# Performance work log

Measured on AMD Instinct MI355X. Metric: run time of the kernel, lower is better.

Reference implementation:

```python
import jax, jax.numpy as jnp
import numpy as np

QMAX = 127.0  # int8 symmetric range


def _quantize(t):
    # per-tensor symmetric int8 quantization
    scale = jnp.maximum(jnp.max(jnp.abs(t)) / QMAX, 1e-8)
    q = jnp.clip(jnp.round(t / scale), -QMAX, QMAX)
    return q, scale


def setup_inputs() -> dict:
    key = jax.random.key(0)
    kx, kw, kb = jax.random.split(key, 3)
    x = jax.random.normal(kx, (32, 128, 56, 56), dtype=jnp.float32)
    weight = jax.random.normal(kw, (256, 128, 3, 3), dtype=jnp.float32) * 0.05
    bias = jax.random.normal(kb, (256,), dtype=jnp.float32) * 0.05
    return {"x": x, "weight": weight, "bias": bias}


def reference(x, weight, bias):
    # Quantize activations and weights to int8 grid (values held in fp32;
    # products are exact small integers, matching int32 GEMM accumulation).
    qx, sx = _quantize(x)
    qw, sw = _quantize(weight)
    # im2col GEMM conv == standard conv on quantized values, int accumulate.
    acc = jax.lax.conv_general_dilated(
        qx, qw,
        window_strides=(1, 1),
        padding=((1, 1), (1, 1)),
        rhs_dilation=(1, 1),
        dimension_numbers=("NCHW", "OIHW", "NCHW"),
    )
    # Dequantize and add bias.
    out = acc * (sx * sw) + bias[None, :, None, None]
    return out
```

## Files before the change

### kernel.cpp

```cpp
#include <hip/hip_runtime.h>
#include <hip/hip_bf16.h>


typedef int v4i __attribute__((ext_vector_type(4)));

#define NBATCH 32
#define CIN    128
#define HW     56
#define PIX    (HW*HW)
#define COUT   256
#define XTOT   (NBATCH*CIN*PIX)
#define WTOT   (COUT*CIN*9)

template <int ITERS>
__global__ __launch_bounds__(256) void absmax_part_kernel(
    const float* __restrict__ in, float* __restrict__ partial)
{
    const float4* in4 = (const float4*)in;
    const int t      = blockIdx.x * 256 + threadIdx.x;
    const int stride = gridDim.x * 256;
    float m = 0.f;
#pragma unroll
    for (int k = 0; k < ITERS; ++k) {
        float4 v = in4[t + k * stride];
        m = fmaxf(m, fmaxf(fmaxf(fabsf(v.x), fabsf(v.y)),
                           fmaxf(fabsf(v.z), fabsf(v.w))));
    }
#pragma unroll
    for (int off = 32; off >= 1; off >>= 1)
        m = fmaxf(m, __shfl_xor(m, off, 64));
    __shared__ float wmax[4];
    const int lane = threadIdx.x & 63, wid = threadIdx.x >> 6;
    if (lane == 0) wmax[wid] = m;
    __syncthreads();
    if (threadIdx.x == 0)
        partial[blockIdx.x] =
            fmaxf(fmaxf(wmax[0], wmax[1]), fmaxf(wmax[2], wmax[3]));
}

__global__ __launch_bounds__(256) void finalize_kernel(
    const float* __restrict__ px, const float* __restrict__ pw,
    float* __restrict__ scales)
{
    const int tid = threadIdx.x;
    float mxv = 0.f, mwv = 0.f;
#pragma unroll
    for (int k = 0; k < 4; ++k) {
        int i = k * 256 + tid;
        if (i < 896) mxv = fmaxf(mxv, px[i]);
    }
    if (tid < 72) mwv = pw[tid];
#pragma unroll
    for (int off = 32; off >= 1; off >>= 1) {
        mxv = fmaxf(mxv, __shfl_xor(mxv, off, 64));
        mwv = fmaxf(mwv, __shfl_xor(mwv, off, 64));
    }
    __shared__ float sx[4], sw[4];
    const int lane = tid & 63, wid = tid >> 6;
    if (lane == 0) { sx[wid] = mxv; sw[wid] = mwv; }
    __syncthreads();
    if (tid == 0) {
        float fx = fmaxf(fmaxf(sx[0], sx[1]), fmaxf(sx[2], sx[3]));
        float fw = fmaxf(fmaxf(sw[0], sw[1]), fmaxf(sw[2], sw[3]));
        scales[0] = fmaxf(fx / 127.0f, 1e-8f);
        scales[1] = fmaxf(fw / 127.0f, 1e-8f);
    }
}

__global__ void quant_w_kernel(const float* __restrict__ w,
                               const float* __restrict__ scales,
                               signed char* __restrict__ qw) {
    float s = scales[1];
    int idx = blockIdx.x * blockDim.x + threadIdx.x;
    if (idx >= WTOT) return;
    int o   = idx / (CIN * 9);
    int rem = idx % (CIN * 9);
    int c   = rem / 9;
    int khw = rem % 9;
    float q = rintf(w[idx] / s);
    q = fminf(127.0f, fmaxf(-127.0f, q));
    qw[khw * (COUT * CIN) + o * CIN + c] = (signed char)(int)q;
}

__global__ __launch_bounds__(256) void quant_x_kernel(const float* __restrict__ x,
                                                      const float* __restrict__ scales,
                                                      signed char* __restrict__ qx) {
    __shared__ signed char lds[32 * 132];
    float s = scales[0];
    const int n   = blockIdx.y;
    const int p0  = blockIdx.x * 32;
    const int tid = threadIdx.x;
#pragma unroll
    for (int i = 0; i < 4; ++i) {
        int idx = i * 256 + tid;
        int c   = idx >> 3;
        int pq  = idx & 7;
        float4 v = *(const float4*)&x[((size_t)(n * CIN + c)) * PIX + p0 + pq * 4];
        float qv[4] = {v.x, v.y, v.z, v.w};
#pragma unroll
        for (int j = 0; j < 4; ++j) {
            float q = rintf(qv[j] / s);
            q = fminf(127.0f, fmaxf(-127.0f, q));
            lds[(pq * 4 + j) * 132 + c] = (signed char)(int)q;
        }
    }
    __syncthreads();
#pragma unroll
    for (int i = 0; i < 4; ++i) {
        int idx = i * 256 + tid;
        int pp  = idx >> 5;
        int cw  = (idx & 31) * 4;
        *(int*)&qx[((size_t)(n * PIX + p0 + pp)) * CIN + cw] =
            *(const int*)&lds[pp * 132 + cw];
    }
}

__global__ __launch_bounds__(256) void conv_kernel(
    const signed char* __restrict__ qx,
    const signed char* __restrict__ qw,
    const float* __restrict__ bias,
    const float* __restrict__ scales,
    float* __restrict__ out)
{
    __shared__ signed char lds[192 * 128];
    const int tid  = threadIdx.x;
    const int lane = tid & 63;
    const int wid  = tid >> 6;
    const int prow = lane & 15;
    const int klo  = lane >> 4;

    const int m0 = blockIdx.x * 64;
    const int n  = m0 / PIX;
    const int p0 = m0 % PIX;

    const size_t xbase = (size_t)n * PIX * CIN;
#pragma unroll
    for (int it = 0; it < 6; ++it) {
        int chunk = it * 256 + tid;
        int r  = chunk >> 3;
        int cb = (chunk & 7) * 16;
        int p  = p0 - 57 + r;
        p = min(max(p, 0), PIX - 1);
        v4i v = *(const v4i*)(qx + xbase + (size_t)p * CIN + (cb ^ ((r & 7) << 4)));
        *(v4i*)&lds[r * 128 + cb] = v;
    }
    __syncthreads();

    v4i acc[4][4] = {};
    const v4i vzero = {0, 0, 0, 0};

    int hh[4], ww[4], rbase[4];
#pragma unroll
    for (int s = 0; s < 4; ++s) {
        int i = s * 16 + prow;
        int p = p0 + i;
        hh[s] = p / HW;
        ww[s] = p % HW;
        rbase[s] = i + 57;
    }

#pragma unroll
    for (int dh = -1; dh <= 1; ++dh) {
#pragma unroll
        for (int dw = -1; dw <= 1; ++dw) {
            const int khw = (dh + 1) * 3 + (dw + 1);
            const signed char* bsrc = qw + (size_t)khw * (COUT * CIN);
#pragma unroll
            for (int kc = 0; kc < 2; ++kc) {
                const int col = kc * 64 + klo * 16;
                v4i b[4];
#pragma unroll
                for (int t = 0; t < 4; ++t) {
                    int ch = wid * 64 + t * 16 + prow;
                    b[t] = *(const v4i*)(bsrc + (size_t)ch * CIN + col);
                }
                v4i a[4];
#pragma unroll
                for (int s = 0; s < 4; ++s) {
                    bool valid = ((unsigned)(hh[s] + dh) < (unsigned)HW) &&
                                 ((unsigned)(ww[s] + dw) < (unsigned)HW);
                    int r = rbase[s] + dh * HW + dw;
                    v4i av = *(const v4i*)&lds[r * 128 + (col ^ ((r & 7) << 4))];
                    a[s] = valid ? av : vzero;
                }
#pragma unroll
                for (int s = 0; s < 4; ++s)
#pragma unroll
                    for (int t = 0; t < 4; ++t)
                        acc[s][t] = __builtin_amdgcn_mfma_i32_16x16x64_i8(
                            a[s], b[t], acc[s][t], 0, 0, 0);
            }
        }
    }

    const float comb = scales[0] * scales[1];
    const size_t obase = (size_t)n * COUT * PIX;
#pragma unroll
    for (int t = 0; t < 4; ++t) {
        int ch = wid * 64 + t * 16 + prow;
        float bs = bias[ch];
#pragma unroll
        for (int s = 0; s < 4; ++s) {
            int p = p0 + s * 16 + klo * 4;
            float4 v;
            v.x = (float)acc[s][t].x * comb + bs;
            v.y = (float)acc[s][t].y * comb + bs;
            v.z = (float)acc[s][t].z * comb + bs;
            v.w = (float)acc[s][t].w * comb + bs;
            *(float4*)&out[obase + (size_t)ch * PIX + p] = v;
        }
    }
}

extern "C" void kernel_launch(void* const* d_in, const int* in_sizes, int n_in,
                              void* d_out, int out_size, void* d_ws, size_t ws_size,
                              hipStream_t stream) {
    const float* x    = (const float*)d_in[0];
    const float* w    = (const float*)d_in[1];
    const float* bias = (const float*)d_in[2];
    float* out = (float*)d_out;

    float*       scales = (float*)d_ws;
    float*       px     = (float*)((char*)d_ws + 1024);
    float*       pw     = (float*)((char*)d_ws + 4608);
    signed char* qx     = (signed char*)d_ws + 8192;
    signed char* qw     = qx + (size_t)XTOT;

    absmax_part_kernel<14><<<896, 256, 0, stream>>>(x, px);
    absmax_part_kernel<4><<<72, 256, 0, stream>>>(w, pw);
    finalize_kernel<<<1, 256, 0, stream>>>(px, pw, scales);
    quant_w_kernel<<<WTOT / 256, 256, 0, stream>>>(w, scales, qw);
    quant_x_kernel<<<dim3(98, 32), 256, 0, stream>>>(x, scales, qx);
    conv_kernel<<<1568, 256, 0, stream>>>(qx, qw, bias, scales, out);
}
```

Before: 226.3 us.

## Split conv output channels across blocks with padded LDS halo and prefetched weights

The conv kernel now splits the 256 output channels into two halves per block, doubling the grid and halving each wave's accumulator count. Occupancy is raised via launch bounds. The input tile is staged in LDS as a zero-padded 58-wide halo, which removes the per-tap boundary checks. Weight fragments are software-prefetched one step ahead. The x absmax reduction also runs on twice as many blocks with fewer iterations each. The trade is that each input tile is loaded twice, once per channel half, and LDS per block grows.

```diff
diff --git a/kernel.cpp b/kernel.cpp
--- a/kernel.cpp
+++ b/kernel.cpp
@@ -45,10 +45,8 @@
     const int tid = threadIdx.x;
     float mxv = 0.f, mwv = 0.f;
 #pragma unroll
-    for (int k = 0; k < 4; ++k) {
-        int i = k * 256 + tid;
-        if (i < 896) mxv = fmaxf(mxv, px[i]);
-    }
+    for (int k = 0; k < 7; ++k)
+        mxv = fmaxf(mxv, px[k * 256 + tid]);
     if (tid < 72) mwv = pw[tid];
 #pragma unroll
     for (int off = 32; off >= 1; off >>= 1) {
@@ -115,89 +113,100 @@
     }
 }
 
-__global__ __launch_bounds__(256) void conv_kernel(
+__global__ __launch_bounds__(256, 4) void conv_kernel(
     const signed char* __restrict__ qx,
     const signed char* __restrict__ qw,
     const float* __restrict__ bias,
     const float* __restrict__ scales,
     float* __restrict__ out)
 {
-    __shared__ signed char lds[192 * 128];
+    __shared__ signed char lds[232 * 128];
     const int tid  = threadIdx.x;
     const int lane = tid & 63;
     const int wid  = tid >> 6;
     const int prow = lane & 15;
     const int klo  = lane >> 4;
 
-    const int m0 = blockIdx.x * 64;
-    const int n  = m0 / PIX;
-    const int p0 = m0 % PIX;
+    const int bid = blockIdx.x;
+    const int nh  = bid & 1;
+    const int mt  = bid >> 1;
+    const int n   = mt / 49;
+    const int p0  = (mt % 49) * 64;
+    const int hbase = p0 / HW - 1;
 
     const size_t xbase = (size_t)n * PIX * CIN;
-#pragma unroll
-    for (int it = 0; it < 6; ++it) {
+
+#pragma unroll
+    for (int it = 0; it < 8; ++it) {
         int chunk = it * 256 + tid;
-        int r  = chunk >> 3;
-        int cb = (chunk & 7) * 16;
-        int p  = p0 - 57 + r;
-        p = min(max(p, 0), PIX - 1);
-        v4i v = *(const v4i*)(qx + xbase + (size_t)p * CIN + (cb ^ ((r & 7) << 4)));
-        *(v4i*)&lds[r * 128 + cb] = v;
-    }
-    __syncthreads();
-
-    v4i acc[4][4] = {};
-    const v4i vzero = {0, 0, 0, 0};
-
-    int hh[4], ww[4], rbase[4];
+        if (chunk < 232 * 8) {
+            int r  = chunk >> 3;
+            int cb = (chunk & 7) * 16;
+            int hr = r / 58;
+            int wc = r - hr * 58;
+            int h  = hbase + hr;
+            int w  = wc - 1;
+            bool valid = ((unsigned)h < HW) && ((unsigned)w < HW);
+            int p = valid ? (h * HW + w) : 0;
+            v4i v = *(const v4i*)(qx + xbase + (size_t)p * CIN + cb);
+            if (!valid) v = (v4i){0, 0, 0, 0};
+            *(v4i*)&lds[r * 128 + (cb ^ ((r & 7) << 4))] = v;
+        }
+    }
+    __syncthreads();
+
+    int rr[4];
 #pragma unroll
     for (int s = 0; s < 4; ++s) {
-        int i = s * 16 + prow;
-        int p = p0 + i;
-        hh[s] = p / HW;
-        ww[s] = p % HW;
-        rbase[s] = i + 57;
-    }
-
-#pragma unroll
-    for (int dh = -1; dh <= 1; ++dh) {
-#pragma unroll
-        for (int dw = -1; dw <= 1; ++dw) {
-            const int khw = (dh + 1) * 3 + (dw + 1);
-            const signed char* bsrc = qw + (size_t)khw * (COUT * CIN);
-#pragma unroll
-            for (int kc = 0; kc < 2; ++kc) {
-                const int col = kc * 64 + klo * 16;
-                v4i b[4];
-#pragma unroll
-                for (int t = 0; t < 4; ++t) {
-                    int ch = wid * 64 + t * 16 + prow;
-                    b[t] = *(const v4i*)(bsrc + (size_t)ch * CIN + col);
-                }
-                v4i a[4];
-#pragma unroll
-                for (int s = 0; s < 4; ++s) {
-                    bool valid = ((unsigned)(hh[s] + dh) < (unsigned)HW) &&
-                                 ((unsigned)(ww[s] + dw) < (unsigned)HW);
-                    int r = rbase[s] + dh * HW + dw;
-                    v4i av = *(const v4i*)&lds[r * 128 + (col ^ ((r & 7) << 4))];
-                    a[s] = valid ? av : vzero;
-                }
-#pragma unroll
-                for (int s = 0; s < 4; ++s)
-#pragma unroll
-                    for (int t = 0; t < 4; ++t)
-                        acc[s][t] = __builtin_amdgcn_mfma_i32_16x16x64_i8(
-                            a[s], b[t], acc[s][t], 0, 0, 0);
-            }
-        }
-    }
-
-    const float comb = scales[0] * scales[1];
+        int p = p0 + s * 16 + prow;
+        int h = p / HW, w = p - h * HW;
+        rr[s] = (h - hbase) * 58 + (w + 1);
+    }
+
+    const int ch0     = nh * 128 + wid * 32;
+    const int colbase = klo * 16;
+
+    v4i acc[4][2] = {};
+
+    const signed char* b0ptr = qw + (size_t)(ch0 + prow) * CIN + colbase;
+#define BADDR(st) (b0ptr + (size_t)((st) >> 1) * (COUT * CIN) + ((st) & 1) * 64)
+
+    v4i bcur0 = *(const v4i*)BADDR(0);
+    v4i bcur1 = *(const v4i*)(BADDR(0) + 16 * CIN);
+
+#pragma unroll
+    for (int st = 0; st < 18; ++st) {
+        v4i bn0 = bcur0, bn1 = bcur1;
+        if (st < 17) {
+            const signed char* bp = BADDR(st + 1);
+            bn0 = *(const v4i*)bp;
+            bn1 = *(const v4i*)(bp + 16 * CIN);
+        }
+        const int khw  = st >> 1;
+        const int rofs = (khw / 3 - 1) * 58 + (khw % 3 - 1);
+        const int col  = (st & 1) * 64 + colbase;
+        v4i a[4];
+#pragma unroll
+        for (int s = 0; s < 4; ++s) {
+            int r = rr[s] + rofs;
+            a[s] = *(const v4i*)&lds[r * 128 + (col ^ ((r & 7) << 4))];
+        }
+#pragma unroll
+        for (int s = 0; s < 4; ++s) {
+            acc[s][0] = __builtin_amdgcn_mfma_i32_16x16x64_i8(a[s], bcur0, acc[s][0], 0, 0, 0);
+            acc[s][1] = __builtin_amdgcn_mfma_i32_16x16x64_i8(a[s], bcur1, acc[s][1], 0, 0, 0);
+        }
+        bcur0 = bn0; bcur1 = bn1;
+    }
+#undef BADDR
+
+    float s0 = scales[0], s1 = scales[1];
+    asm volatile("" : "+v"(s0));
+    const float comb = s0 * s1;
     const size_t obase = (size_t)n * COUT * PIX;
 #pragma unroll
-    for (int t = 0; t < 4; ++t) {
-        int ch = wid * 64 + t * 16 + prow;
+    for (int t = 0; t < 2; ++t) {
+        int ch = ch0 + t * 16 + prow;
         float bs = bias[ch];
 #pragma unroll
         for (int s = 0; s < 4; ++s) {
@@ -221,15 +230,15 @@
     float* out = (float*)d_out;
 
     float*       scales = (float*)d_ws;
-    float*       px     = (float*)((char*)d_ws + 1024);
-    float*       pw     = (float*)((char*)d_ws + 4608);
+    float*       px     = (float*)((char*)d_ws + 256);
+    float*       pw     = (float*)((char*)d_ws + 7680);
     signed char* qx     = (signed char*)d_ws + 8192;
     signed char* qw     = qx + (size_t)XTOT;
 
-    absmax_part_kernel<14><<<896, 256, 0, stream>>>(x, px);
+    absmax_part_kernel<7><<<1792, 256, 0, stream>>>(x, px);
     absmax_part_kernel<4><<<72, 256, 0, stream>>>(w, pw);
     finalize_kernel<<<1, 256, 0, stream>>>(px, pw, scales);
     quant_w_kernel<<<WTOT / 256, 256, 0, stream>>>(w, scales, qw);
     quant_x_kernel<<<dim3(98, 32), 256, 0, stream>>>(x, scales, qx);
-    conv_kernel<<<1568, 256, 0, stream>>>(qx, qw, bias, scales, out);
-}
+    conv_kernel<<<3136, 256, 0, stream>>>(qx, qw, bias, scales, out);
+}
```

Result: faster. 217.9 us (-3.7%).
